# Optimization experiments

Measured on AMD Instinct MI355X. Metric: run time of the kernel, lower is better.

The kernel has to match this reference:

```python
import jax, jax.numpy as jnp
import numpy as np
from jax import lax

VOCAB = 32000
H = 1024
T = 4096


def setup_inputs() -> dict:
    key = jax.random.key(0)
    ks = jax.random.split(key, 6)
    s = 1.0 / np.sqrt(H)  # PyTorch GRU init scale
    x = jax.random.randint(ks[0], (T,), 0, VOCAB)
    embedding = jax.random.normal(ks[1], (VOCAB, H), dtype=jnp.float32)
    # direction 0 = 'forward', direction 1 = 'reverse' (both run left-to-right
    # here because the original feeds one timestep at a time)
    w_ih = jax.random.uniform(ks[2], (2, 3 * H, H), jnp.float32, -s, s)
    w_hh = jax.random.uniform(ks[3], (2, 3 * H, H), jnp.float32, -s, s)
    b_ih = jax.random.uniform(ks[4], (2, 3 * H), jnp.float32, -s, s)
    b_hh = jax.random.uniform(ks[5], (2, 3 * H), jnp.float32, -s, s)
    return {"x": x, "embedding": embedding, "w_ih": w_ih, "w_hh": w_hh,
            "b_ih": b_ih, "b_hh": b_hh}


def reference(x, embedding, w_ih, w_hh, b_ih, b_hh):
    emb = embedding[x]  # (T, H)
    # Precompute input-side gate projections for both directions: (T, 2, 3H)
    x_proj = jnp.einsum('th,dgh->tdg', emb, w_ih) + b_ih

    def step(h, xp):  # h: (2, H), xp: (2, 3H)
        hp = jnp.einsum('dh,dgh->dg', h, w_hh) + b_hh  # (2, 3H)
        xr, xz, xn = xp[:, :H], xp[:, H:2 * H], xp[:, 2 * H:]
        hr, hz, hn = hp[:, :H], hp[:, H:2 * H], hp[:, 2 * H:]
        r = jax.nn.sigmoid(xr + hr)
        z = jax.nn.sigmoid(xz + hz)
        n = jnp.tanh(xn + r * hn)
        h_new = (1.0 - z) * n + z * h
        return h_new, h_new

    h0 = jnp.zeros((2, H), emb.dtype)
    h_last, hs = lax.scan(step, h0, x_proj)  # hs: (T, 2, H)
    # per-step output = concat(dir0_hidden, dir1_hidden) -> (T, 2H)
    outputs = hs.reshape(T, 2 * H)
    # final hidden = sum of the two direction hiddens, shape (1, H)
    hidden = (h_last[0] + h_last[1])[None, :]
    return outputs, hidden
```

## Files before the change

kernel.cpp:

```cpp
#include <hip/hip_runtime.h>
#include <hip/hip_bf16.h>
#include <stdint.h>

#define HDIM 1024
#define TSEQ 4096
#define GATES3 3072
#define NTOT 6144

typedef __attribute__((ext_vector_type(8))) short short8;
typedef __attribute__((ext_vector_type(4))) float f32x4;

__device__ __forceinline__ unsigned short f2bf(float f) {
    uint32_t u = __float_as_uint(f);
    uint32_t r = (u + 0x7FFFu + ((u >> 16) & 1u)) >> 16;
    return (unsigned short)r;
}
__device__ __forceinline__ float bf2f(unsigned short s) {
    return __uint_as_float(((uint32_t)s) << 16);
}

__global__ __launch_bounds__(256) void init_tags_kernel(unsigned long long* __restrict__ comm) {
    int i = blockIdx.x * 256 + threadIdx.x;
    comm[(size_t)i * 8] = 0xFFFFFFFFFFFFFFFFull;
}

__global__ __launch_bounds__(256) void xproj_gemm_kernel(
    const int* __restrict__ x, const float* __restrict__ emb,
    const float* __restrict__ w_ih, const float* __restrict__ b_ih,
    unsigned short* __restrict__ rz, float* __restrict__ n32)
{
    __shared__ short As[128][32];
    __shared__ short Bs[128][32];

    const int tid = threadIdx.x;
    const int m0 = blockIdx.x * 128;
    const int n0 = blockIdx.y * 128;

    const int srow = tid >> 1;
    const int half = tid & 1;

    const int arow_g = x[m0 + srow];
    const float* aptr = emb + (size_t)arow_g * HDIM + half * 16;
    const float* bptr = w_ih + (size_t)(n0 + srow) * HDIM + half * 16;

    const int wid = tid >> 6;
    const int lane = tid & 63;
    const int wm = wid >> 1;
    const int wn = wid & 1;
    const int l15 = lane & 15;
    const int ksel = (lane >> 4) * 8;

    f32x4 acc[4][4];
    f32x4 zero4 = {0.f, 0.f, 0.f, 0.f};
#pragma unroll
    for (int mi = 0; mi < 4; mi++)
#pragma unroll
        for (int ni = 0; ni < 4; ni++) acc[mi][ni] = zero4;

    for (int k0 = 0; k0 < HDIM; k0 += 32) {
        float4 av[4], bv[4];
#pragma unroll
        for (int jj = 0; jj < 4; jj++) {
            av[jj] = *(const float4*)(aptr + k0 + jj * 4);
            bv[jj] = *(const float4*)(bptr + k0 + jj * 4);
        }
        if (k0) __syncthreads();
        short ta[16], tb[16];
#pragma unroll
        for (int jj = 0; jj < 4; jj++) {
            ta[jj*4+0] = f2bf(av[jj].x); ta[jj*4+1] = f2bf(av[jj].y);
            ta[jj*4+2] = f2bf(av[jj].z); ta[jj*4+3] = f2bf(av[jj].w);
            tb[jj*4+0] = f2bf(bv[jj].x); tb[jj*4+1] = f2bf(bv[jj].y);
            tb[jj*4+2] = f2bf(bv[jj].z); tb[jj*4+3] = f2bf(bv[jj].w);
        }
        *(short8*)&As[srow][half * 16]     = *(short8*)&ta[0];
        *(short8*)&As[srow][half * 16 + 8] = *(short8*)&ta[8];
        *(short8*)&Bs[srow][half * 16]     = *(short8*)&tb[0];
        *(short8*)&Bs[srow][half * 16 + 8] = *(short8*)&tb[8];
        __syncthreads();

        short8 af[4], bfr[4];
#pragma unroll
        for (int mi = 0; mi < 4; mi++)
            af[mi] = *(const short8*)&As[wm * 64 + mi * 16 + l15][ksel];
#pragma unroll
        for (int ni = 0; ni < 4; ni++)
            bfr[ni] = *(const short8*)&Bs[wn * 64 + ni * 16 + l15][ksel];
#pragma unroll
        for (int mi = 0; mi < 4; mi++)
#pragma unroll
            for (int ni = 0; ni < 4; ni++)
                acc[mi][ni] = __builtin_amdgcn_mfma_f32_16x16x32_bf16(
                    af[mi], bfr[ni], acc[mi][ni], 0, 0, 0);
    }

    const int r0 = m0 + wm * 64;
    const int c0 = n0 + wn * 64;
#pragma unroll
    for (int mi = 0; mi < 4; mi++) {
#pragma unroll
        for (int ni = 0; ni < 4; ni++) {
            int c = c0 + ni * 16 + l15;
            int dir = (c >= GATES3) ? 1 : 0;
            int g3 = c - dir * GATES3;
            int gate = g3 >> 10;
            int jj = g3 & 1023;
            float bias = b_ih[c];
#pragma unroll
            for (int v = 0; v < 4; v++) {
                int r = r0 + mi * 16 + (lane >> 4) * 4 + v;
                float val = acc[mi][ni][v] + bias;
                if (gate < 2)
                    rz[(size_t)r * 4096 + dir * 2048 + gate * 1024 + jj] = f2bf(val);
                else
                    n32[(size_t)r * 2048 + dir * 1024 + jj] = val;
            }
        }
    }
}

__global__ __launch_bounds__(256, 1) void rnn_kernel(
    const unsigned short* __restrict__ rz, const float* __restrict__ n32,
    const float* __restrict__ w_hh, const float* __restrict__ b_hh,
    unsigned long long* __restrict__ comm, float* __restrict__ out)
{
    __shared__ float h_lds[2][1056];

    const int tid = threadIdx.x;
    const int bid = blockIdx.x;
    const int dir = bid >> 7;
    const int wg  = bid & 127;
    const int j0  = wg * 8;
    const int g   = tid >> 5;
    const int sl  = tid & 31;
    const int j   = j0 + g;

    float4 w0[8], w1[8], w2[8];
    {
        const float* Wd = w_hh + (size_t)dir * GATES3 * HDIM;
        const float* wp0 = Wd + ((size_t)(0 * HDIM + j)) * HDIM + sl * 32;
        const float* wp1 = Wd + ((size_t)(1 * HDIM + j)) * HDIM + sl * 32;
        const float* wp2 = Wd + ((size_t)(2 * HDIM + j)) * HDIM + sl * 32;
#pragma unroll
        for (int c4 = 0; c4 < 8; c4++) {
            w0[c4] = *(const float4*)(wp0 + c4 * 4);
            w1[c4] = *(const float4*)(wp1 + c4 * 4);
            w2[c4] = *(const float4*)(wp2 + c4 * 4);
        }
    }
    float bh0 = 0.f, bh1 = 0.f, bh2 = 0.f;
    if (sl == 0) {
        bh0 = b_hh[dir * GATES3 + j];
        bh1 = b_hh[dir * GATES3 + HDIM + j];
        bh2 = b_hh[dir * GATES3 + 2 * HDIM + j];
    }

    const unsigned long long* c00 = comm + ((size_t)(0 * 2 + dir) * 1024 + tid) * 8;
    const unsigned long long* c01 = c00 + 256 * 8;
    const unsigned long long* c02 = c00 + 512 * 8;
    const unsigned long long* c03 = c00 + 768 * 8;
    const unsigned long long* c10 = comm + ((size_t)(1 * 2 + dir) * 1024 + tid) * 8;
    const unsigned long long* c11 = c10 + 256 * 8;
    const unsigned long long* c12 = c10 + 512 * 8;
    const unsigned long long* c13 = c10 + 768 * 8;

    unsigned long long* sp0 = comm + ((size_t)(0 * 2 + dir) * 1024 + j) * 8;
    unsigned long long* sp1 = comm + ((size_t)(1 * 2 + dir) * 1024 + j) * 8;

    const int idx0 = tid + (tid >> 5);
    const unsigned short* rzp = rz + dir * 2048 + j;
    const float* np = n32 + dir * 1024 + j;
    uint32_t* orow = (uint32_t*)out + dir * HDIM + j;

    float last_h = 0.f;

    for (int t = 0; t < TSEQ; t++) {
        const int buf = t & 1;

        float xr = 0.f, xz = 0.f, xn = 0.f;
        if (sl == 0) {
            xr = bf2f(rzp[0]);
            xz = bf2f(rzp[1024]);
            xn = np[0];
        }
        rzp += 4096; np += 2048;

        if (t == 0) {
            h_lds[0][idx0]       = 0.f;
            h_lds[0][idx0 + 264] = 0.f;
            h_lds[0][idx0 + 528] = 0.f;
            h_lds[0][idx0 + 792] = 0.f;
        } else {
            const uint32_t want = (uint32_t)(t - 1);
            const int pp = (t - 1) & 1;
            const unsigned long long* q0 = pp ? c10 : c00;
            const unsigned long long* q1 = pp ? c11 : c01;
            const unsigned long long* q2 = pp ? c12 : c02;
            const unsigned long long* q3 = pp ? c13 : c03;
            unsigned long long v0 = 0, v1 = 0, v2 = 0, v3 = 0;
            bool d0 = false, d1 = false, d2 = false, d3 = false;
            do {
                unsigned long long t0 = 0, t1 = 0, t2 = 0, t3 = 0;
                if (!d0) t0 = __hip_atomic_load(q0, __ATOMIC_RELAXED, __HIP_MEMORY_SCOPE_AGENT);
                if (!d1) t1 = __hip_atomic_load(q1, __ATOMIC_RELAXED, __HIP_MEMORY_SCOPE_AGENT);
                if (!d2) t2 = __hip_atomic_load(q2, __ATOMIC_RELAXED, __HIP_MEMORY_SCOPE_AGENT);
                if (!d3) t3 = __hip_atomic_load(q3, __ATOMIC_RELAXED, __HIP_MEMORY_SCOPE_AGENT);
                if (!d0 && (uint32_t)t0 == want) { v0 = t0; d0 = true; }
                if (!d1 && (uint32_t)t1 == want) { v1 = t1; d1 = true; }
                if (!d2 && (uint32_t)t2 == want) { v2 = t2; d2 = true; }
                if (!d3 && (uint32_t)t3 == want) { v3 = t3; d3 = true; }
            } while (!(d0 && d1 && d2 && d3));
            h_lds[buf][idx0]       = __uint_as_float((uint32_t)(v0 >> 32));
            h_lds[buf][idx0 + 264] = __uint_as_float((uint32_t)(v1 >> 32));
            h_lds[buf][idx0 + 528] = __uint_as_float((uint32_t)(v2 >> 32));
            h_lds[buf][idx0 + 792] = __uint_as_float((uint32_t)(v3 >> 32));
        }
        __syncthreads();

        float a0 = 0.f, a1 = 0.f, a2 = 0.f;
#pragma unroll
        for (int c4 = 0; c4 < 8; c4++) {
            float4 hv = *(const float4*)&h_lds[buf][sl * 33 + c4 * 4];
            a0 += w0[c4].x*hv.x + w0[c4].y*hv.y + w0[c4].z*hv.z + w0[c4].w*hv.w;
            a1 += w1[c4].x*hv.x + w1[c4].y*hv.y + w1[c4].z*hv.z + w1[c4].w*hv.w;
            a2 += w2[c4].x*hv.x + w2[c4].y*hv.y + w2[c4].z*hv.z + w2[c4].w*hv.w;
        }
#pragma unroll
        for (int m = 1; m < 32; m <<= 1) {
            a0 += __shfl_xor(a0, m, 32);
            a1 += __shfl_xor(a1, m, 32);
            a2 += __shfl_xor(a2, m, 32);
        }

        if (sl == 0) {
            float r  = 1.f / (1.f + __expf(-(xr + a0 + bh0)));
            float z  = 1.f / (1.f + __expf(-(xz + a1 + bh1)));
            float y  = xn + r * (a2 + bh2);
            float e2 = __expf(2.f * y);
            float n_ = 1.f - 2.f / (e2 + 1.f);
            float hp = h_lds[buf][j + (j >> 5)];
            float hnew = z * (hp - n_) + n_;
            last_h = hnew;
            unsigned long long pack =
                ((unsigned long long)__float_as_uint(hnew) << 32) | (uint32_t)t;
            __hip_atomic_store((t & 1) ? sp1 : sp0, pack,
                               __ATOMIC_RELAXED, __HIP_MEMORY_SCOPE_AGENT);
            orow[0] = __float_as_uint(hnew);
        }
        orow += 2 * HDIM;
    }

    if (dir == 0 && sl == 0) {
        const unsigned long long* q = comm + ((size_t)(1 * 2 + 1) * 1024 + j) * 8;
        unsigned long long v;
        do {
            v = __hip_atomic_load(q, __ATOMIC_RELAXED, __HIP_MEMORY_SCOPE_AGENT);
        } while ((uint32_t)v != (uint32_t)(TSEQ - 1));
        out[(size_t)TSEQ * 2 * HDIM + j] = last_h + __uint_as_float((uint32_t)(v >> 32));
    }
}

extern "C" void kernel_launch(void* const* d_in, const int* in_sizes, int n_in,
                              void* d_out, int out_size, void* d_ws, size_t ws_size,
                              hipStream_t stream)
{
    const int*   x     = (const int*)d_in[0];
    const float* emb   = (const float*)d_in[1];
    const float* w_ih  = (const float*)d_in[2];
    const float* w_hh  = (const float*)d_in[3];
    const float* b_ih  = (const float*)d_in[4];
    const float* b_hh  = (const float*)d_in[5];
    float* out = (float*)d_out;

    unsigned short* rz  = (unsigned short*)d_ws;
    float* n32 = (float*)((char*)d_ws + (size_t)TSEQ * 4096 * 2);
    unsigned long long* comm =
        (unsigned long long*)((char*)d_ws + (size_t)TSEQ * 4096 * 2 + (size_t)TSEQ * 2048 * 4);

    init_tags_kernel<<<16, 256, 0, stream>>>(comm);

    dim3 g(TSEQ / 128, NTOT / 128);
    xproj_gemm_kernel<<<g, 256, 0, stream>>>(x, emb, w_ih, b_ih, rz, n32);

    const unsigned short* a0 = rz;
    const float* a1 = n32;
    const float* a2 = w_hh;
    const float* a3 = b_hh;
    unsigned long long* a4 = comm;
    float* a5 = out;
    void* args[] = { (void*)&a0, (void*)&a1, (void*)&a2, (void*)&a3, (void*)&a4, (void*)&a5 };
    hipLaunchCooperativeKernel((void*)rnn_kernel, dim3(256), dim3(256), args, 0, stream);
}
```

Measured before the change: 8.535 ms.

## Repartition GRU recurrence to 64 blocks with packed 16-byte polled handoff

The recurrent kernel moves from 256 blocks of 256 threads to 64 blocks of 512 threads, each owning 32 hidden units with 16 lanes per unit and 64 weights per lane held in registers. The hidden-state exchange drops the padded per-slot 64-byte tags and packs tag/value pairs densely, so each thread polls one 16-byte system-coherent load carrying two values instead of four separate atomic loads. Per-step output rows are written coalesced from LDS by a few threads one step late, and the final hidden sum gets its own flag array. Fewer communicating blocks and fewer polled cache lines should cut per-step sync latency, but each block does 4x more FMA work per step and register pressure rises.

```diff
diff --git a/kernel.cpp b/kernel.cpp
--- a/kernel.cpp
+++ b/kernel.cpp
@@ -7,8 +7,12 @@
 #define GATES3 3072
 #define NTOT 6144
 
+#define COMM_OFF (64u * 1024 * 1024)
+#define XFIN_OFF (COMM_OFF + 32768)
+
 typedef __attribute__((ext_vector_type(8))) short short8;
 typedef __attribute__((ext_vector_type(4))) float f32x4;
+typedef __attribute__((ext_vector_type(4))) unsigned int ux4;
 
 __device__ __forceinline__ unsigned short f2bf(float f) {
     uint32_t u = __float_as_uint(f);
@@ -19,9 +23,19 @@
     return __uint_as_float(((uint32_t)s) << 16);
 }
 
-__global__ __launch_bounds__(256) void init_tags_kernel(unsigned long long* __restrict__ comm) {
+__device__ __forceinline__ ux4 ld16_sys(const void* p) {
+    ux4 r;
+    asm volatile("global_load_dwordx4 %0, %1, off sc0 sc1\n\ts_waitcnt vmcnt(0)"
+                 : "=v"(r) : "v"(p) : "memory");
+    return r;
+}
+
+__global__ __launch_bounds__(256) void init_comm_kernel(uint8_t* __restrict__ wsb) {
     int i = blockIdx.x * 256 + threadIdx.x;
-    comm[(size_t)i * 8] = 0xFFFFFFFFFFFFFFFFull;
+    unsigned long long* comm = (unsigned long long*)(wsb + COMM_OFF);
+    unsigned long long* xfin = (unsigned long long*)(wsb + XFIN_OFF);
+    if (i < 4096) comm[i] = ~0ull;
+    if (i < 1024) xfin[i] = ~0ull;
 }
 
 __global__ __launch_bounds__(256) void xproj_gemm_kernel(
@@ -119,33 +133,35 @@
     }
 }
 
-__global__ __launch_bounds__(256, 1) void rnn_kernel(
+__global__ __launch_bounds__(512, 1) void rnn_kernel(
     const unsigned short* __restrict__ rz, const float* __restrict__ n32,
     const float* __restrict__ w_hh, const float* __restrict__ b_hh,
-    unsigned long long* __restrict__ comm, float* __restrict__ out)
+    uint8_t* __restrict__ wsb, float* __restrict__ out)
 {
-    __shared__ float h_lds[2][1056];
+    __shared__ float h_lds[2][1088];
+
+    uint8_t* comm = wsb + COMM_OFF;
+    unsigned long long* xfin = (unsigned long long*)(wsb + XFIN_OFF);
 
     const int tid = threadIdx.x;
     const int bid = blockIdx.x;
-    const int dir = bid >> 7;
-    const int wg  = bid & 127;
-    const int j0  = wg * 8;
-    const int g   = tid >> 5;
-    const int sl  = tid & 31;
-    const int j   = j0 + g;
-
-    float4 w0[8], w1[8], w2[8];
+    const int dir = bid >> 5;
+    const int role = bid & 31;
+    const int g   = tid >> 4;
+    const int sl  = tid & 15;
+    const int j   = role * 32 + g;
+
+    f32x4 w0[16], w1[16], w2[16];
     {
         const float* Wd = w_hh + (size_t)dir * GATES3 * HDIM;
-        const float* wp0 = Wd + ((size_t)(0 * HDIM + j)) * HDIM + sl * 32;
-        const float* wp1 = Wd + ((size_t)(1 * HDIM + j)) * HDIM + sl * 32;
-        const float* wp2 = Wd + ((size_t)(2 * HDIM + j)) * HDIM + sl * 32;
-#pragma unroll
-        for (int c4 = 0; c4 < 8; c4++) {
-            w0[c4] = *(const float4*)(wp0 + c4 * 4);
-            w1[c4] = *(const float4*)(wp1 + c4 * 4);
-            w2[c4] = *(const float4*)(wp2 + c4 * 4);
+        const float* p0 = Wd + ((size_t)(0 * HDIM + j)) * HDIM + sl * 64;
+        const float* p1 = Wd + ((size_t)(1 * HDIM + j)) * HDIM + sl * 64;
+        const float* p2 = Wd + ((size_t)(2 * HDIM + j)) * HDIM + sl * 64;
+#pragma unroll
+        for (int c4 = 0; c4 < 16; c4++) {
+            w0[c4] = *(const f32x4*)(p0 + c4 * 4);
+            w1[c4] = *(const f32x4*)(p1 + c4 * 4);
+            w2[c4] = *(const f32x4*)(p2 + c4 * 4);
         }
     }
     float bh0 = 0.f, bh1 = 0.f, bh2 = 0.f;
@@ -155,22 +171,17 @@
         bh2 = b_hh[dir * GATES3 + 2 * HDIM + j];
     }
 
-    const unsigned long long* c00 = comm + ((size_t)(0 * 2 + dir) * 1024 + tid) * 8;
-    const unsigned long long* c01 = c00 + 256 * 8;
-    const unsigned long long* c02 = c00 + 512 * 8;
-    const unsigned long long* c03 = c00 + 768 * 8;
-    const unsigned long long* c10 = comm + ((size_t)(1 * 2 + dir) * 1024 + tid) * 8;
-    const unsigned long long* c11 = c10 + 256 * 8;
-    const unsigned long long* c12 = c10 + 512 * 8;
-    const unsigned long long* c13 = c10 + 768 * 8;
-
-    unsigned long long* sp0 = comm + ((size_t)(0 * 2 + dir) * 1024 + j) * 8;
-    unsigned long long* sp1 = comm + ((size_t)(1 * 2 + dir) * 1024 + j) * 8;
-
-    const int idx0 = tid + (tid >> 5);
+    uint8_t* commD = comm + dir * 8192;
+    const uint8_t* poll0 = commD + (size_t)tid * 16;
+    const uint8_t* poll1 = poll0 + 16384;
+    unsigned long long* slot0 = (unsigned long long*)(commD) + j;
+    unsigned long long* slot1 = (unsigned long long*)(commD + 16384) + j;
+
+    const int idx0 = 2 * tid + 4 * (tid >> 5);
     const unsigned short* rzp = rz + dir * 2048 + j;
     const float* np = n32 + dir * 1024 + j;
-    uint32_t* orow = (uint32_t*)out + dir * HDIM + j;
+    const int ocol = role * 32 + 2 * tid;
+    const int oidx = ocol + 4 * (ocol >> 6);
 
     float last_h = 0.f;
 
@@ -186,50 +197,40 @@
         rzp += 4096; np += 2048;
 
         if (t == 0) {
-            h_lds[0][idx0]       = 0.f;
-            h_lds[0][idx0 + 264] = 0.f;
-            h_lds[0][idx0 + 528] = 0.f;
-            h_lds[0][idx0 + 792] = 0.f;
+            h_lds[0][idx0]     = 0.f;
+            h_lds[0][idx0 + 1] = 0.f;
         } else {
             const uint32_t want = (uint32_t)(t - 1);
-            const int pp = (t - 1) & 1;
-            const unsigned long long* q0 = pp ? c10 : c00;
-            const unsigned long long* q1 = pp ? c11 : c01;
-            const unsigned long long* q2 = pp ? c12 : c02;
-            const unsigned long long* q3 = pp ? c13 : c03;
-            unsigned long long v0 = 0, v1 = 0, v2 = 0, v3 = 0;
-            bool d0 = false, d1 = false, d2 = false, d3 = false;
-            do {
-                unsigned long long t0 = 0, t1 = 0, t2 = 0, t3 = 0;
-                if (!d0) t0 = __hip_atomic_load(q0, __ATOMIC_RELAXED, __HIP_MEMORY_SCOPE_AGENT);
-                if (!d1) t1 = __hip_atomic_load(q1, __ATOMIC_RELAXED, __HIP_MEMORY_SCOPE_AGENT);
-                if (!d2) t2 = __hip_atomic_load(q2, __ATOMIC_RELAXED, __HIP_MEMORY_SCOPE_AGENT);
-                if (!d3) t3 = __hip_atomic_load(q3, __ATOMIC_RELAXED, __HIP_MEMORY_SCOPE_AGENT);
-                if (!d0 && (uint32_t)t0 == want) { v0 = t0; d0 = true; }
-                if (!d1 && (uint32_t)t1 == want) { v1 = t1; d1 = true; }
-                if (!d2 && (uint32_t)t2 == want) { v2 = t2; d2 = true; }
-                if (!d3 && (uint32_t)t3 == want) { v3 = t3; d3 = true; }
-            } while (!(d0 && d1 && d2 && d3));
-            h_lds[buf][idx0]       = __uint_as_float((uint32_t)(v0 >> 32));
-            h_lds[buf][idx0 + 264] = __uint_as_float((uint32_t)(v1 >> 32));
-            h_lds[buf][idx0 + 528] = __uint_as_float((uint32_t)(v2 >> 32));
-            h_lds[buf][idx0 + 792] = __uint_as_float((uint32_t)(v3 >> 32));
+            const uint8_t* src = ((t - 1) & 1) ? poll1 : poll0;
+            ux4 v;
+            do { v = ld16_sys(src); } while (v.x != want || v.z != want);
+            h_lds[buf][idx0]     = __uint_as_float(v.y);
+            h_lds[buf][idx0 + 1] = __uint_as_float(v.w);
         }
         __syncthreads();
 
-        float a0 = 0.f, a1 = 0.f, a2 = 0.f;
-#pragma unroll
-        for (int c4 = 0; c4 < 8; c4++) {
-            float4 hv = *(const float4*)&h_lds[buf][sl * 33 + c4 * 4];
-            a0 += w0[c4].x*hv.x + w0[c4].y*hv.y + w0[c4].z*hv.z + w0[c4].w*hv.w;
-            a1 += w1[c4].x*hv.x + w1[c4].y*hv.y + w1[c4].z*hv.z + w1[c4].w*hv.w;
-            a2 += w2[c4].x*hv.x + w2[c4].y*hv.y + w2[c4].z*hv.z + w2[c4].w*hv.w;
-        }
-#pragma unroll
-        for (int m = 1; m < 32; m <<= 1) {
-            a0 += __shfl_xor(a0, m, 32);
-            a1 += __shfl_xor(a1, m, 32);
-            a2 += __shfl_xor(a2, m, 32);
+        if (t > 0 && tid < 16) {
+            float2 hv = *(float2*)&h_lds[buf][oidx];
+            *(float2*)(out + (size_t)(t - 1) * 2048 + dir * 1024 + ocol) = hv;
+        }
+
+        f32x4 s0 = {0,0,0,0}, s1 = {0,0,0,0}, s2 = {0,0,0,0};
+        const float* hb = &h_lds[buf][sl * 68];
+#pragma unroll
+        for (int c4 = 0; c4 < 16; c4++) {
+            f32x4 hv = *(const f32x4*)(hb + c4 * 4);
+            s0 += w0[c4] * hv;
+            s1 += w1[c4] * hv;
+            s2 += w2[c4] * hv;
+        }
+        float a0 = s0.x + s0.y + s0.z + s0.w;
+        float a1 = s1.x + s1.y + s1.z + s1.w;
+        float a2 = s2.x + s2.y + s2.z + s2.w;
+#pragma unroll
+        for (int m = 1; m < 16; m <<= 1) {
+            a0 += __shfl_xor(a0, m, 16);
+            a1 += __shfl_xor(a1, m, 16);
+            a2 += __shfl_xor(a2, m, 16);
         }
 
         if (sl == 0) {
@@ -238,25 +239,30 @@
             float y  = xn + r * (a2 + bh2);
             float e2 = __expf(2.f * y);
             float n_ = 1.f - 2.f / (e2 + 1.f);
-            float hp = h_lds[buf][j + (j >> 5)];
+            float hp = h_lds[buf][j + 4 * (j >> 6)];
             float hnew = z * (hp - n_) + n_;
             last_h = hnew;
             unsigned long long pack =
                 ((unsigned long long)__float_as_uint(hnew) << 32) | (uint32_t)t;
-            __hip_atomic_store((t & 1) ? sp1 : sp0, pack,
+            __hip_atomic_store((t & 1) ? slot1 : slot0, pack,
                                __ATOMIC_RELAXED, __HIP_MEMORY_SCOPE_AGENT);
-            orow[0] = __float_as_uint(hnew);
-        }
-        orow += 2 * HDIM;
-    }
-
+        }
+    }
+
+    if (sl == 0)
+        out[(size_t)(TSEQ - 1) * 2048 + dir * 1024 + j] = last_h;
+
+    if (dir == 1 && sl == 0) {
+        unsigned long long pack =
+            ((unsigned long long)__float_as_uint(last_h) << 32) | 0x0BADF00Du;
+        __hip_atomic_store(&xfin[j], pack, __ATOMIC_RELAXED, __HIP_MEMORY_SCOPE_AGENT);
+    }
     if (dir == 0 && sl == 0) {
-        const unsigned long long* q = comm + ((size_t)(1 * 2 + 1) * 1024 + j) * 8;
         unsigned long long v;
         do {
-            v = __hip_atomic_load(q, __ATOMIC_RELAXED, __HIP_MEMORY_SCOPE_AGENT);
-        } while ((uint32_t)v != (uint32_t)(TSEQ - 1));
-        out[(size_t)TSEQ * 2 * HDIM + j] = last_h + __uint_as_float((uint32_t)(v >> 32));
+            v = __hip_atomic_load(&xfin[j], __ATOMIC_RELAXED, __HIP_MEMORY_SCOPE_AGENT);
+        } while ((uint32_t)v != 0x0BADF00Du);
+        out[(size_t)TSEQ * 2048 + j] = last_h + __uint_as_float((uint32_t)(v >> 32));
     }
 }
 
@@ -274,10 +280,9 @@
 
     unsigned short* rz  = (unsigned short*)d_ws;
     float* n32 = (float*)((char*)d_ws + (size_t)TSEQ * 4096 * 2);
-    unsigned long long* comm =
-        (unsigned long long*)((char*)d_ws + (size_t)TSEQ * 4096 * 2 + (size_t)TSEQ * 2048 * 4);
-
-    init_tags_kernel<<<16, 256, 0, stream>>>(comm);
+    uint8_t* wsb = (uint8_t*)d_ws;
+
+    init_comm_kernel<<<16, 256, 0, stream>>>(wsb);
 
     dim3 g(TSEQ / 128, NTOT / 128);
     xproj_gemm_kernel<<<g, 256, 0, stream>>>(x, emb, w_ih, b_ih, rz, n32);
@@ -286,8 +291,8 @@
     const float* a1 = n32;
     const float* a2 = w_hh;
     const float* a3 = b_hh;
-    unsigned long long* a4 = comm;
+    uint8_t* a4 = wsb;
     float* a5 = out;
     void* args[] = { (void*)&a0, (void*)&a1, (void*)&a2, (void*)&a3, (void*)&a4, (void*)&a5 };
-    hipLaunchCooperativeKernel((void*)rnn_kernel, dim3(256), dim3(256), args, 0, stream);
-}
+    hipLaunchCooperativeKernel((void*)rnn_kernel, dim3(64), dim3(512), args, 0, stream);
+}
```

New measurement: 7.797 ms. -8.6%, faster.
